# Optimization experiments

Measured on AMD Instinct MI355X. Metric: run time of the kernel, lower is better.

## Reference

```python
import jax, jax.numpy as jnp
import numpy as np

NEG_SLOPE = 0.2  # PyG GATConv default negative_slope


def gat_conv(x, edge_index, W, att_src, att_dst, bias):
    # PyG GATConv, heads=1, add_self_loops=True, lin bias=False, final bias added
    N = x.shape[0]
    h = x @ W                                     # [N, F]
    loops = jnp.arange(N, dtype=edge_index.dtype)
    src = jnp.concatenate([edge_index[0], loops])
    dst = jnp.concatenate([edge_index[1], loops])
    a_src = h @ att_src                           # [N]
    a_dst = h @ att_dst                           # [N]
    e = a_src[src] + a_dst[dst]
    e = jnp.where(e > 0, e, NEG_SLOPE * e)        # leaky_relu
    m = jax.ops.segment_max(e, dst, num_segments=N)
    w = jnp.exp(e - m[dst])
    denom = jax.ops.segment_sum(w, dst, num_segments=N)
    alpha = w / denom[dst]
    out = jax.ops.segment_sum(h[src] * alpha[:, None], dst, num_segments=N)
    return out + bias


def gcn_conv(x, edge_index, W, b):
    # PyG GCNConv: add self-loops + symmetric normalization
    N = x.shape[0]
    loops = jnp.arange(N, dtype=edge_index.dtype)
    src = jnp.concatenate([edge_index[0], loops])
    dst = jnp.concatenate([edge_index[1], loops])
    deg = jax.ops.segment_sum(jnp.ones(src.shape[0], dtype=x.dtype), dst, num_segments=N)
    dinv = jax.lax.rsqrt(jnp.maximum(deg, 1e-12))  # deg >= 1 thanks to self-loops
    norm = dinv[src] * dinv[dst]
    xw = x @ W
    return jax.ops.segment_sum(xw[src] * norm[:, None], dst, num_segments=N) + b


def get_final_node(x, batch, num_graphs):
    nn_ = jax.ops.segment_sum(jnp.ones(x.shape[0], dtype=jnp.int32), batch, num_segments=num_graphs)
    cum = jnp.concatenate([jnp.zeros(1, dtype=nn_.dtype), jnp.cumsum(nn_)[:-1]])
    return x[cum]


def ontology_emb(table, e1, e2, W, asrc, adst, b, idx_map):
    emb = gat_conv(table, e1, W, asrc, adst, b)
    emb = gat_conv(emb, e2, W, asrc, adst, b)
    return emb[idx_map]


def _forward(spec_emb, diag_table, proce_table, atc_table,
             diag_W, diag_asrc, diag_adst, diag_b,
             proce_W, proce_asrc, proce_adst, proce_b,
             atc_W, atc_asrc, atc_adst, atc_b,
             gcn_W1, gcn_b1, gcn_W2, gcn_b2, gcn_W3, gcn_b3,
             diag_e1, diag_e2, proce_e1, proce_e2, atc_e1, atc_e2,
             diag_map, proce_map, atc_map,
             left_x, left_graph_index, right_x, right_graph_index,
             left_x_batch, right_x_batch, num_graphs):
    diag_emb = ontology_emb(diag_table, diag_e1, diag_e2, diag_W, diag_asrc, diag_adst, diag_b, diag_map)
    proce_emb = ontology_emb(proce_table, proce_e1, proce_e2, proce_W, proce_asrc, proce_adst, proce_b, proce_map)
    atc_emb = ontology_emb(atc_table, atc_e1, atc_e2, atc_W, atc_asrc, atc_adst, atc_b, atc_map)
    all_emb = jnp.concatenate([spec_emb, diag_emb, proce_emb, atc_emb], axis=0)
    lh = all_emb[left_x[:, 0]]   # squeeze(dim=1)
    rh = all_emb[right_x[:, 0]]
    for W, b in ((gcn_W1, gcn_b1), (gcn_W2, gcn_b2), (gcn_W3, gcn_b3)):
        lh = gcn_conv(lh, left_graph_index, W, b)
        rh = gcn_conv(rh, right_graph_index, W, b)
    lf = get_final_node(lh, left_x_batch, num_graphs)
    rf = get_final_node(rh, right_x_batch, num_graphs)
    eps = 1e-6  # CosineSimilarity eps
    num = jnp.sum(lf * rf, axis=-1)
    den = jnp.maximum(jnp.linalg.norm(lf, axis=-1), eps) * jnp.maximum(jnp.linalg.norm(rf, axis=-1), eps)
    return num / den


def setup_inputs() -> dict:
    key = jax.random.key(0)
    ks = jax.random.split(key, 32)
    HID = 128
    B, NPG = 2048, 50
    N = B * NPG               # 102400 nodes per side
    E_PAT = 409600            # 4 edges per node
    DIAG_N, DIAG_L = 30000, 20000
    PROCE_N, PROCE_L = 12000, 8000
    ATC_N, ATC_L = 6000, 4000
    ALL = 1 + DIAG_L + PROCE_L + ATC_L
    f = lambda k, s: jax.random.normal(k, s, dtype=jnp.float32)
    scale = 0.1
    inp = {
        'spec_emb': f(ks[0], (1, HID)),
        'diag_table': f(ks[1], (DIAG_N, HID)),
        'proce_table': f(ks[2], (PROCE_N, HID)),
        'atc_table': f(ks[3], (ATC_N, HID)),
    }
    for i, nm in enumerate(['diag', 'proce', 'atc']):
        inp[nm + '_W'] = f(ks[4 + i], (HID, HID)) * scale
        inp[nm + '_asrc'] = f(ks[7 + i], (HID,)) * scale
        inp[nm + '_adst'] = f(ks[10 + i], (HID,)) * scale
        inp[nm + '_b'] = jnp.zeros((HID,), jnp.float32)
    for j in range(3):
        inp['gcn_W%d' % (j + 1)] = f(ks[13 + j], (HID, HID)) * scale
        inp['gcn_b%d' % (j + 1)] = jnp.zeros((HID,), jnp.float32)
    inp['diag_e1'] = jax.random.randint(ks[16], (2, DIAG_N), 0, DIAG_N, dtype=jnp.int32)
    inp['diag_e2'] = jax.random.randint(ks[17], (2, DIAG_N), 0, DIAG_N, dtype=jnp.int32)
    inp['proce_e1'] = jax.random.randint(ks[18], (2, PROCE_N), 0, PROCE_N, dtype=jnp.int32)
    inp['proce_e2'] = jax.random.randint(ks[19], (2, PROCE_N), 0, PROCE_N, dtype=jnp.int32)
    inp['atc_e1'] = jax.random.randint(ks[20], (2, ATC_N), 0, ATC_N, dtype=jnp.int32)
    inp['atc_e2'] = jax.random.randint(ks[21], (2, ATC_N), 0, ATC_N, dtype=jnp.int32)
    inp['diag_map'] = jnp.arange(DIAG_L, dtype=jnp.int32)
    inp['proce_map'] = jnp.arange(PROCE_L, dtype=jnp.int32)
    inp['atc_map'] = jnp.arange(ATC_L, dtype=jnp.int32)
    inp['left_x'] = jax.random.randint(ks[22], (N, 1), 0, ALL, dtype=jnp.int32)
    inp['right_x'] = jax.random.randint(ks[23], (N, 1), 0, ALL, dtype=jnp.int32)
    inp['left_graph_index'] = jax.random.randint(ks[24], (2, E_PAT), 0, N, dtype=jnp.int32)
    inp['right_graph_index'] = jax.random.randint(ks[25], (2, E_PAT), 0, N, dtype=jnp.int32)
    batch = jnp.repeat(jnp.arange(B, dtype=jnp.int32), NPG)
    inp['left_x_batch'] = batch
    inp['right_x_batch'] = batch
    inp['num_graphs'] = B
    return inp


def reference(spec_emb, diag_table, proce_table, atc_table,
              diag_W, diag_asrc, diag_adst, diag_b,
              proce_W, proce_asrc, proce_adst, proce_b,
              atc_W, atc_asrc, atc_adst, atc_b,
              gcn_W1, gcn_b1, gcn_W2, gcn_b2, gcn_W3, gcn_b3,
              diag_e1, diag_e2, proce_e1, proce_e2, atc_e1, atc_e2,
              diag_map, proce_map, atc_map,
              left_x, left_graph_index, right_x, right_graph_index,
              left_x_batch, right_x_batch, num_graphs):
    return _forward(spec_emb, diag_table, proce_table, atc_table,
                    diag_W, diag_asrc, diag_adst, diag_b,
                    proce_W, proce_asrc, proce_adst, proce_b,
                    atc_W, atc_asrc, atc_adst, atc_b,
                    gcn_W1, gcn_b1, gcn_W2, gcn_b2, gcn_W3, gcn_b3,
                    diag_e1, diag_e2, proce_e1, proce_e2, atc_e1, atc_e2,
                    diag_map, proce_map, atc_map,
                    left_x, left_graph_index, right_x, right_graph_index,
                    left_x_batch, right_x_batch, num_graphs)
```

## Files before the change

kernel.cpp:

```cpp
#include <hip/hip_runtime.h>
#include <hip/hip_bf16.h>

#define HID 128

typedef unsigned int uint;
typedef unsigned short ushort;
typedef short short8 __attribute__((ext_vector_type(8)));
typedef float f32x4 __attribute__((ext_vector_type(4)));

static inline int cdiv_i(long a, long b) { return (int)((a + b - 1) / b); }

__device__ __forceinline__ float bf2f(uint hi) {
    return __builtin_bit_cast(float, hi << 16);
}
__device__ __forceinline__ ushort f2bf(float f) {
    uint u = __builtin_bit_cast(uint, f);
    u = (u + 0x7fffu + ((u >> 16) & 1u)) >> 16;
    return (ushort)u;
}

__global__ void build_aug(const float* __restrict__ W1, const float* __restrict__ b1,
                          const float* __restrict__ b2,
                          float* __restrict__ aug1, float* __restrict__ aug2) {
    const int i = blockIdx.x * 256 + threadIdx.x;
    if (i < 128 * 128) aug1[i] = W1[i];
    else if (i < 129 * 128) aug1[i] = b1[i - 128 * 128];
    if (i < 128) aug2[129 * 128 + i] = b2[i];
}

__global__ void matmul128f(const float* __restrict__ A, const float* __restrict__ B,
                           float* __restrict__ C, int M) {
    const int idx = blockIdx.x * 256 + threadIdx.x;
    if (idx >= M * 128) return;
    const int i = idx >> 7, j = idx & 127;
    float s = 0.f;
#pragma unroll 8
    for (int k = 0; k < 128; ++k) s += A[i * 128 + k] * B[k * 128 + j];
    C[idx] = s;
}

struct W4 { const float* w[4]; };

__global__ void wtrans_k(W4 ws, ushort* __restrict__ out) {
    const int idx = blockIdx.x * 256 + threadIdx.x;
    if (idx >= 4 * 16384) return;
    const int m = idx >> 14;
    const int e = idx & 16383;
    const int n = e >> 7, k = e & 127;
    out[idx] = f2bf(ws.w[m][k * 128 + n]);
}

__device__ __forceinline__ void stage_wt(const ushort* __restrict__ Wt,
                                         ushort* __restrict__ wl) {
    const int t = threadIdx.x;
    const int row = t >> 1, half = (t & 1) * 64;
    const uint4* src = (const uint4*)(Wt + row * 128 + half);
    uint4* dst = (uint4*)(wl + row * 136 + half);
#pragma unroll
    for (int i = 0; i < 8; ++i) dst[i] = src[i];
}

template <typename AT>
__device__ __forceinline__ void load_afrag(const AT* __restrict__ A, long row,
                                           int koff, short8& af) {
    if constexpr (__is_same(AT, ushort)) {
        const uint4 raw = *(const uint4*)(A + row * 128 + koff);
        af = __builtin_bit_cast(short8, raw);
    } else {
        const float4* p = (const float4*)(A + row * 128 + koff);
        const float4 x0 = p[0], x1 = p[1];
        af[0] = (short)f2bf(x0.x); af[1] = (short)f2bf(x0.y);
        af[2] = (short)f2bf(x0.z); af[3] = (short)f2bf(x0.w);
        af[4] = (short)f2bf(x1.x); af[5] = (short)f2bf(x1.y);
        af[6] = (short)f2bf(x1.z); af[7] = (short)f2bf(x1.w);
    }
}

template <typename AT, typename OT>
__device__ __forceinline__ void mfma_tile(const AT* __restrict__ A,
                                          const ushort* __restrict__ wl,
                                          const float* __restrict__ bias,
                                          OT* __restrict__ C,
                                          long m0blk, long rowEnd) {
    const int tid = threadIdx.x;
    const int wave = tid >> 6, lane = tid & 63;
    const int r = lane & 15, q = lane >> 4;
    const long m0 = m0blk + wave * 32;

    f32x4 acc[2][8];
#pragma unroll
    for (int mi = 0; mi < 2; ++mi)
#pragma unroll
        for (int ni = 0; ni < 8; ++ni) acc[mi][ni] = (f32x4)0.f;

#pragma unroll
    for (int t = 0; t < 4; ++t) {
        const int koff = t * 32 + q * 8;
        short8 bfr[8];
#pragma unroll
        for (int ni = 0; ni < 8; ++ni) {
            const uint4 raw = *(const uint4*)(&wl[(ni * 16 + r) * 136 + koff]);
            bfr[ni] = __builtin_bit_cast(short8, raw);
        }
#pragma unroll
        for (int mi = 0; mi < 2; ++mi) {
            long row = m0 + mi * 16 + r;
            if (row >= rowEnd) row = rowEnd - 1;
            short8 af;
            load_afrag<AT>(A, row, koff, af);
#pragma unroll
            for (int ni = 0; ni < 8; ++ni)
                acc[mi][ni] = __builtin_amdgcn_mfma_f32_16x16x32_bf16(
                    af, bfr[ni], acc[mi][ni], 0, 0, 0);
        }
    }

#pragma unroll
    for (int mi = 0; mi < 2; ++mi) {
#pragma unroll
        for (int ni = 0; ni < 8; ++ni) {
            const int col = ni * 16 + r;
            const float bv = bias ? bias[col] : 0.f;
#pragma unroll
            for (int reg = 0; reg < 4; ++reg) {
                const long row = m0 + mi * 16 + q * 4 + reg;
                if (row < rowEnd) {
                    const float v = acc[mi][ni][reg] + bv;
                    if constexpr (__is_same(OT, ushort))
                        C[row * 128 + col] = f2bf(v);
                    else
                        C[row * 128 + col] = v;
                }
            }
        }
    }
}

template <typename OT>
__global__ __launch_bounds__(256) void gemm_gcn(const ushort* __restrict__ A,
                                                const ushort* __restrict__ Wt,
                                                const float* __restrict__ bias,
                                                OT* __restrict__ C, int M) {
    __shared__ ushort wl[128 * 136];
    stage_wt(Wt, wl);
    __syncthreads();
    const long m0 = (long)blockIdx.x * 256;
    mfma_tile<ushort, OT>(A, wl, bias, C, m0, M);
    if (m0 + 128 < M)
        mfma_tile<ushort, OT>(A, wl, bias, C, m0 + 128, M);
}

struct GOnto {
    const ushort* Wt0; const ushort* Wt1; const ushort* Wt2;
    const float* s0; const float* s1; const float* s2;
    const float* d0; const float* d1; const float* d2;
    int bs1, bs2;
    int r1, r2, r3;
};

template <typename AT>
__global__ __launch_bounds__(256) void gemm_onto(const AT* x0, const AT* x1,
                                                 const AT* x2, GOnto g,
                                                 ushort* __restrict__ H,
                                                 float* __restrict__ as_o,
                                                 float* __restrict__ ad_o) {
    __shared__ ushort wl[128 * 136];
    const int b = blockIdx.x;
    const int gid = (b >= g.bs1) + (b >= g.bs2);
    const ushort* Wt = (gid == 0) ? g.Wt0 : (gid == 1) ? g.Wt1 : g.Wt2;
    const float* avs = (gid == 0) ? g.s0 : (gid == 1) ? g.s1 : g.s2;
    const float* avd = (gid == 0) ? g.d0 : (gid == 1) ? g.d1 : g.d2;
    const AT* Ag = (gid == 0) ? x0 : (gid == 1) ? x1 : x2;
    const int bloc = b - ((gid == 0) ? 0 : (gid == 1) ? g.bs1 : g.bs2);
    const long rb = (gid == 0) ? 0 : (gid == 1) ? g.r1 : g.r2;
    const long Mg = ((gid == 0) ? g.r1 : (gid == 1) ? g.r2 : g.r3) - rb;
    stage_wt(Wt, wl);
    __syncthreads();

    const int tid = threadIdx.x;
    const int wave = tid >> 6, lane = tid & 63;
    const int r = lane & 15, q = lane >> 4;
    const long m0 = (long)bloc * 128 + wave * 32;

    f32x4 acc[2][8];
#pragma unroll
    for (int mi = 0; mi < 2; ++mi)
#pragma unroll
        for (int ni = 0; ni < 8; ++ni) acc[mi][ni] = (f32x4)0.f;

#pragma unroll
    for (int t = 0; t < 4; ++t) {
        const int koff = t * 32 + q * 8;
        short8 bfr[8];
#pragma unroll
        for (int ni = 0; ni < 8; ++ni) {
            const uint4 raw = *(const uint4*)(&wl[(ni * 16 + r) * 136 + koff]);
            bfr[ni] = __builtin_bit_cast(short8, raw);
        }
#pragma unroll
        for (int mi = 0; mi < 2; ++mi) {
            long row = m0 + mi * 16 + r;
            if (row >= Mg) row = Mg - 1;
            short8 af;
            load_afrag<AT>(Ag, row, koff, af);
#pragma unroll
            for (int ni = 0; ni < 8; ++ni)
                acc[mi][ni] = __builtin_amdgcn_mfma_f32_16x16x32_bf16(
                    af, bfr[ni], acc[mi][ni], 0, 0, 0);
        }
    }

    ushort* Hg = H + rb * 128;
#pragma unroll
    for (int mi = 0; mi < 2; ++mi) {
#pragma unroll
        for (int ni = 0; ni < 8; ++ni) {
            const int col = ni * 16 + r;
#pragma unroll
            for (int reg = 0; reg < 4; ++reg) {
                const long row = m0 + mi * 16 + q * 4 + reg;
                if (row < Mg) Hg[row * 128 + col] = f2bf(acc[mi][ni][reg]);
            }
        }
    }

    float asv[8], adv[8];
#pragma unroll
    for (int ni = 0; ni < 8; ++ni) {
        asv[ni] = avs[ni * 16 + r];
        adv[ni] = avd[ni * 16 + r];
    }
#pragma unroll
    for (int mi = 0; mi < 2; ++mi) {
#pragma unroll
        for (int reg = 0; reg < 4; ++reg) {
            float ps = 0.f, pd = 0.f;
#pragma unroll
            for (int ni = 0; ni < 8; ++ni) {
                ps += acc[mi][ni][reg] * asv[ni];
                pd += acc[mi][ni][reg] * adv[ni];
            }
#pragma unroll
            for (int o = 1; o < 16; o <<= 1) {
                ps += __shfl_xor(ps, o);
                pd += __shfl_xor(pd, o);
            }
            const long row = m0 + mi * 16 + q * 4 + reg;
            if (r == 0 && row < Mg) {
                as_o[rb + row] = ps;
                ad_o[rb + row] = pd;
            }
        }
    }
}

struct GatP {
    int r1, r2;
    int ob0, ob1, ob2;
    const float* b0; const float* b1; const float* b2;
};

__device__ __forceinline__ void acc8(float* acc, float w, const uint4 v) {
    acc[0] += w * bf2f(v.x & 0xffff);
    acc[1] += w * bf2f(v.x >> 16);
    acc[2] += w * bf2f(v.y & 0xffff);
    acc[3] += w * bf2f(v.y >> 16);
    acc[4] += w * bf2f(v.z & 0xffff);
    acc[5] += w * bf2f(v.z >> 16);
    acc[6] += w * bf2f(v.w & 0xffff);
    acc[7] += w * bf2f(v.w >> 16);
}

__global__ __launch_bounds__(256) void gat_all(const ushort* __restrict__ h,
                                               const float* __restrict__ as,
                                               const float* __restrict__ ad,
                                               const int* __restrict__ offs,
                                               const int* __restrict__ srcl,
                                               GatP p, ushort* __restrict__ out,
                                               int Mtot) {
    const int node = blockIdx.x * 16 + (threadIdx.x >> 4);
    const int ql = threadIdx.x & 15;
    if (node >= Mtot) return;
    const int gid = (node >= p.r1) + (node >= p.r2);
    const int rb = (gid == 0) ? 0 : (gid == 1) ? p.r1 : p.r2;
    const int ob = (gid == 0) ? p.ob0 : (gid == 1) ? p.ob1 : p.ob2;
    const float* bias = (gid == 0) ? p.b0 : (gid == 1) ? p.b1 : p.b2;
    const int local = node - rb;
    const int beg = offs[ob + local], end = offs[ob + local + 1];
    const float adv = ad[node];
    float m = -1e30f;
    for (int j = beg; j < end; ++j) {
        float e = as[rb + srcl[j]] + adv;
        e = (e > 0.f) ? e : 0.2f * e;
        m = fmaxf(m, e);
    }
    float denom = 0.f;
    float acc[8] = {0.f, 0.f, 0.f, 0.f, 0.f, 0.f, 0.f, 0.f};
    int j = beg;
    for (; j + 2 <= end; j += 2) {
        const int s0 = srcl[j], s1 = srcl[j + 1];
        float e0 = as[rb + s0] + adv; e0 = (e0 > 0.f) ? e0 : 0.2f * e0;
        float e1 = as[rb + s1] + adv; e1 = (e1 > 0.f) ? e1 : 0.2f * e1;
        const float w0 = __expf(e0 - m), w1 = __expf(e1 - m);
        const uint4 v0 = *(const uint4*)(h + (size_t)(rb + s0) * 128 + ql * 8);
        const uint4 v1 = *(const uint4*)(h + (size_t)(rb + s1) * 128 + ql * 8);
        denom += w0 + w1;
        acc8(acc, w0, v0);
        acc8(acc, w1, v1);
    }
    if (j < end) {
        const int s0 = srcl[j];
        float e0 = as[rb + s0] + adv; e0 = (e0 > 0.f) ? e0 : 0.2f * e0;
        const float w0 = __expf(e0 - m);
        const uint4 v0 = *(const uint4*)(h + (size_t)(rb + s0) * 128 + ql * 8);
        denom += w0;
        acc8(acc, w0, v0);
    }
    const float inv = 1.f / denom;
    const float4 bv0 = *(const float4*)(bias + ql * 8);
    const float4 bv1 = *(const float4*)(bias + ql * 8 + 4);
    uint4 o;
    o.x = (uint)f2bf(acc[0] * inv + bv0.x) | ((uint)f2bf(acc[1] * inv + bv0.y) << 16);
    o.y = (uint)f2bf(acc[2] * inv + bv0.z) | ((uint)f2bf(acc[3] * inv + bv0.w) << 16);
    o.z = (uint)f2bf(acc[4] * inv + bv1.x) | ((uint)f2bf(acc[5] * inv + bv1.y) << 16);
    o.w = (uint)f2bf(acc[6] * inv + bv1.z) | ((uint)f2bf(acc[7] * inv + bv1.w) << 16);
    *(uint4*)(out + (size_t)node * 128 + ql * 8) = o;
}

struct CsrDesc {
    const int* esrc[8];
    const int* edst[8];
    int ebase[9];
    int nbase[9];
    int totE;
};

__global__ void csr_count_b(CsrDesc d, int* __restrict__ cnt, int* __restrict__ pos) {
    const int i = blockIdx.x * 256 + threadIdx.x;
    if (i >= d.totE) return;
    int li = 0;
#pragma unroll
    for (int k = 1; k < 8; ++k) li += (i >= d.ebase[k]);
    const int v = d.nbase[li] + d.edst[li][i - d.ebase[li]];
    pos[i] = atomicAdd(&cnt[v], 1);
}

__global__ void csr_fill_b(CsrDesc d, const int* __restrict__ offs,
                           const int* __restrict__ pos, const int* __restrict__ cnt,
                           int* __restrict__ srcl, int4* __restrict__ pedge,
                           const float* __restrict__ dinv,
                           const int* __restrict__ lx, const int* __restrict__ rx,
                           int NP, int NV, int pB) {
    const int i = blockIdx.x * 256 + threadIdx.x;
    int v, s, li, idx;
    if (i < d.totE) {
        li = 0;
#pragma unroll
        for (int k = 1; k < 8; ++k) li += (i >= d.ebase[k]);
        const int j = i - d.ebase[li];
        v = d.nbase[li] + d.edst[li][j];
        s = d.esrc[li][j];
        idx = offs[v] + pos[i];
    } else if (i < d.totE + NV) {
        v = i - d.totE;
        li = 0;
#pragma unroll
        for (int k = 1; k < 8; ++k) li += (v >= d.nbase[k]);
        s = v - d.nbase[li];
        idx = offs[v] + cnt[v];
    } else return;
    if (li >= 6) {
        const int sg = (li - 6) * NP + s;
        int4 rec;
        rec.x = sg;
        rec.y = (li == 7 ? rx : lx)[s];
        rec.z = __float_as_int(dinv[v - d.nbase[6]] * dinv[sg]);
        rec.w = 0;
        pedge[idx - pB] = rec;
    } else {
        srcl[idx] = s;
    }
}

__global__ void first_node(const int* __restrict__ bL, const int* __restrict__ bR,
                           int NP, int* __restrict__ gfL, int* __restrict__ gfR) {
    const int i = blockIdx.x * 256 + threadIdx.x;
    if (i >= 2 * NP) return;
    const int side = i >= NP;
    const int ii = i - (side ? NP : 0);
    const int* b = side ? bR : bL;
    int* gf = side ? gfR : gfL;
    const int cur = b[ii];
    const int prev = (ii == 0) ? -1 : b[ii - 1];
    for (int g = prev + 1; g <= cur; ++g) gf[g] = ii;
}

__global__ __launch_bounds__(1024) void scan_tile(const int* __restrict__ in,
                                                  int* __restrict__ out,
                                                  int* __restrict__ bsum, int n,
                                                  int pn0, int pcnt,
                                                  float* __restrict__ dinv) {
    __shared__ int buf[1024];
    const int tid = threadIdx.x;
    const int i = blockIdx.x * 1024 + tid;
    const int v = (i < n) ? (in[i] + 1) : 0;
    if (i >= pn0 && i < pn0 + pcnt)
        dinv[i - pn0] = rsqrtf(fmaxf((float)v, 1e-12f));
    buf[tid] = v;
    __syncthreads();
    int x = v;
    for (int o = 1; o < 1024; o <<= 1) {
        const int t = (tid >= o) ? buf[tid - o] : 0;
        __syncthreads();
        x += t;
        buf[tid] = x;
        __syncthreads();
    }
    if (i < n) out[i] = x - v;
    if (tid == 1023) bsum[blockIdx.x] = x;
}

__global__ __launch_bounds__(1024) void scan_single(int* __restrict__ bsum, int nb) {
    __shared__ int buf[1024];
    const int tid = threadIdx.x;
    const int v = (tid < nb) ? bsum[tid] : 0;
    buf[tid] = v;
    __syncthreads();
    int x = v;
    for (int o = 1; o < 1024; o <<= 1) {
        const int t = (tid >= o) ? buf[tid - o] : 0;
        __syncthreads();
        x += t;
        buf[tid] = x;
        __syncthreads();
    }
    if (tid < nb) bsum[tid] = x - v;
    if (tid == 1023) bsum[nb] = x;
}

__global__ void scan_add(int* __restrict__ out, const int* __restrict__ bsum,
                         int n, int nb) {
    const int i = blockIdx.x * 256 + threadIdx.x;
    if (i < n) out[i] += bsum[i >> 10];
    else if (i == n) out[i] = bsum[nb];
}

struct EmbD {
    const float* spec; const ushort* oE;
    const int* m0; const int* m1; const int* m2;
    int lb2, lb3;
    int r1, r2;
    long ALLr;
};

__global__ void build_emb(EmbD d, ushort* __restrict__ out) {
    const long t = (long)blockIdx.x * 256 + threadIdx.x;
    if (t >= d.ALLr * 16) return;
    const int row = (int)(t >> 4), c = (int)(t & 15);
    uint4 o;
    if (row == 0) {
        const float4 f0 = ((const float4*)d.spec)[c * 2];
        const float4 f1 = ((const float4*)d.spec)[c * 2 + 1];
        o.x = (uint)f2bf(f0.x) | ((uint)f2bf(f0.y) << 16);
        o.y = (uint)f2bf(f0.z) | ((uint)f2bf(f0.w) << 16);
        o.z = (uint)f2bf(f1.x) | ((uint)f2bf(f1.y) << 16);
        o.w = (uint)f2bf(f1.z) | ((uint)f2bf(f1.w) << 16);
    } else {
        const int seg = (row >= d.lb2) + (row >= d.lb3);
        const int local = row - ((seg == 0) ? 1 : (seg == 1) ? d.lb2 : d.lb3);
        const int* mp = (seg == 0) ? d.m0 : (seg == 1) ? d.m1 : d.m2;
        const int rb = (seg == 0) ? 0 : (seg == 1) ? d.r1 : d.r2;
        o = ((const uint4*)(d.oE + (size_t)(rb + mp[local]) * 128))[c];
    }
    ((uint4*)out)[(size_t)row * 16 + c] = o;
}

__global__ __launch_bounds__(256) void gcn_agg1(const ushort* __restrict__ A3,
                                                const int4* __restrict__ pedge,
                                                const int* __restrict__ offs6,
                                                const float* __restrict__ c1,
                                                ushort* __restrict__ t1,
                                                int NP2, int pB) {
    const int n2 = blockIdx.x * 16 + (threadIdx.x >> 4);
    const int ql = threadIdx.x & 15;
    if (n2 >= NP2) return;
    const int beg = offs6[n2] - pB, end = offs6[n2 + 1] - pB;
    float acc[8] = {0.f, 0.f, 0.f, 0.f, 0.f, 0.f, 0.f, 0.f};
    int j = beg;
    for (; j + 2 <= end; j += 2) {
        const int4 r0 = pedge[j], r1 = pedge[j + 1];
        const float w0 = __int_as_float(r0.z), w1 = __int_as_float(r1.z);
        const uint4 v0 = *(const uint4*)(A3 + (size_t)r0.y * 128 + ql * 8);
        const uint4 v1 = *(const uint4*)(A3 + (size_t)r1.y * 128 + ql * 8);
        acc8(acc, w0, v0);
        acc8(acc, w1, v1);
    }
    if (j < end) {
        const int4 r0 = pedge[j];
        const uint4 v0 = *(const uint4*)(A3 + (size_t)r0.y * 128 + ql * 8);
        acc8(acc, __int_as_float(r0.z), v0);
    }
    const float4 bv0 = *(const float4*)(c1 + ql * 8);
    const float4 bv1 = *(const float4*)(c1 + ql * 8 + 4);
    uint4 o;
    o.x = (uint)f2bf(acc[0] + bv0.x) | ((uint)f2bf(acc[1] + bv0.y) << 16);
    o.y = (uint)f2bf(acc[2] + bv0.z) | ((uint)f2bf(acc[3] + bv0.w) << 16);
    o.z = (uint)f2bf(acc[4] + bv1.x) | ((uint)f2bf(acc[5] + bv1.y) << 16);
    o.w = (uint)f2bf(acc[6] + bv1.z) | ((uint)f2bf(acc[7] + bv1.w) << 16);
    *(uint4*)(t1 + (size_t)n2 * 128 + ql * 8) = o;
}

__device__ __forceinline__ void gcn_q_acc(const ushort* __restrict__ x,
                                          const int4* __restrict__ pedge,
                                          int beg, int end, int ql, float* acc) {
    int j = beg;
    for (; j + 2 <= end; j += 2) {
        const int4 r0 = pedge[j], r1 = pedge[j + 1];
        const float w0 = __int_as_float(r0.z), w1 = __int_as_float(r1.z);
        const uint4 v0 = *(const uint4*)(x + (size_t)r0.x * 128 + ql * 8);
        const uint4 v1 = *(const uint4*)(x + (size_t)r1.x * 128 + ql * 8);
        acc8(acc, w0, v0);
        acc8(acc, w1, v1);
    }
    if (j < end) {
        const int4 r0 = pedge[j];
        const uint4 v0 = *(const uint4*)(x + (size_t)r0.x * 128 + ql * 8);
        acc8(acc, __int_as_float(r0.z), v0);
    }
}

__global__ __launch_bounds__(256) void gcn_agg2(const ushort* __restrict__ t1,
                                                const int4* __restrict__ pedge,
                                                const int* __restrict__ offs6,
                                                const float* __restrict__ c2,
                                                ushort* __restrict__ t2,
                                                int NP2, int pB) {
    const int n2 = blockIdx.x * 16 + (threadIdx.x >> 4);
    const int ql = threadIdx.x & 15;
    if (n2 >= NP2) return;
    const int beg = offs6[n2] - pB, end = offs6[n2 + 1] - pB;
    float acc[8] = {0.f, 0.f, 0.f, 0.f, 0.f, 0.f, 0.f, 0.f};
    gcn_q_acc(t1, pedge, beg, end, ql, acc);
    const float4 bv0 = *(const float4*)(c2 + ql * 8);
    const float4 bv1 = *(const float4*)(c2 + ql * 8 + 4);
    uint4 o;
    o.x = (uint)f2bf(acc[0] + bv0.x) | ((uint)f2bf(acc[1] + bv0.y) << 16);
    o.y = (uint)f2bf(acc[2] + bv0.z) | ((uint)f2bf(acc[3] + bv0.w) << 16);
    o.z = (uint)f2bf(acc[4] + bv1.x) | ((uint)f2bf(acc[5] + bv1.y) << 16);
    o.w = (uint)f2bf(acc[6] + bv1.z) | ((uint)f2bf(acc[7] + bv1.w) << 16);
    *(uint4*)(t2 + (size_t)n2 * 128 + ql * 8) = o;
}

__global__ __launch_bounds__(256) void gcn_final(const ushort* __restrict__ t2,
                                                 const int4* __restrict__ pedge,
                                                 const int* __restrict__ offs6,
                                                 const int* __restrict__ gfL,
                                                 const int* __restrict__ gfR,
                                                 const float* __restrict__ b3,
                                                 float* __restrict__ lfrf,
                                                 int B, int NP, int pB) {
    const int g2 = blockIdx.x * 16 + (threadIdx.x >> 4);
    const int ql = threadIdx.x & 15;
    if (g2 >= 2 * B) return;
    const int side = g2 >= B;
    const int gl = g2 - (side ? B : 0);
    const int n2 = (side ? NP : 0) + (side ? gfR : gfL)[gl];
    const int beg = offs6[n2] - pB, end = offs6[n2 + 1] - pB;
    float acc[8] = {0.f, 0.f, 0.f, 0.f, 0.f, 0.f, 0.f, 0.f};
    gcn_q_acc(t2, pedge, beg, end, ql, acc);
    const float4 bv0 = *(const float4*)(b3 + ql * 8);
    const float4 bv1 = *(const float4*)(b3 + ql * 8 + 4);
    float* op = lfrf + (size_t)g2 * 128 + ql * 8;
    op[0] = acc[0] + bv0.x; op[1] = acc[1] + bv0.y;
    op[2] = acc[2] + bv0.z; op[3] = acc[3] + bv0.w;
    op[4] = acc[4] + bv1.x; op[5] = acc[5] + bv1.y;
    op[6] = acc[6] + bv1.z; op[7] = acc[7] + bv1.w;
}

__global__ __launch_bounds__(256) void cosine_k(const float* __restrict__ lfrf,
                                                float* __restrict__ out, int B) {
    const int g = blockIdx.x * 4 + (threadIdx.x >> 6);
    const int lane = threadIdx.x & 63;
    if (g >= B) return;
    const float2 a = *(const float2*)(lfrf + (size_t)g * 128 + lane * 2);
    const float2 b = *(const float2*)(lfrf + (size_t)(B + g) * 128 + lane * 2);
    float num = a.x * b.x + a.y * b.y;
    float na = a.x * a.x + a.y * a.y;
    float nb = b.x * b.x + b.y * b.y;
#pragma unroll
    for (int o = 32; o > 0; o >>= 1) {
        num += __shfl_down(num, o);
        na += __shfl_down(na, o);
        nb += __shfl_down(nb, o);
    }
    if (lane == 0)
        out[g] = num / (fmaxf(sqrtf(na), 1e-6f) * fmaxf(sqrtf(nb), 1e-6f));
}

extern "C" void kernel_launch(void* const* d_in, const int* in_sizes, int n_in,
                              void* d_out, int out_size, void* d_ws, size_t ws_size,
                              hipStream_t stream) {
    (void)n_in; (void)ws_size;
    const float* spec = (const float*)d_in[0];
    const float* tabs[3] = {(const float*)d_in[1], (const float*)d_in[2], (const float*)d_in[3]};
    const float* ontW[3] = {(const float*)d_in[4], (const float*)d_in[8], (const float*)d_in[12]};
    const float* ontAs[3] = {(const float*)d_in[5], (const float*)d_in[9], (const float*)d_in[13]};
    const float* ontAd[3] = {(const float*)d_in[6], (const float*)d_in[10], (const float*)d_in[14]};
    const float* ontB[3] = {(const float*)d_in[7], (const float*)d_in[11], (const float*)d_in[15]};
    const float* gcnW[3] = {(const float*)d_in[16], (const float*)d_in[18], (const float*)d_in[20]};
    const float* gcnB[3] = {(const float*)d_in[17], (const float*)d_in[19], (const float*)d_in[21]};
    const int* e1s[3] = {(const int*)d_in[22], (const int*)d_in[24], (const int*)d_in[26]};
    const int* e2s[3] = {(const int*)d_in[23], (const int*)d_in[25], (const int*)d_in[27]};
    const int* maps[3] = {(const int*)d_in[28], (const int*)d_in[29], (const int*)d_in[30]};
    const int* left_x = (const int*)d_in[31];
    const int* right_x = (const int*)d_in[32];
    const int* left_eg = (const int*)d_in[33];
    const int* right_eg = (const int*)d_in[34];
    const int* left_batch = (const int*)d_in[35];
    const int* right_batch = (const int*)d_in[36];

    int Ms[3] = {in_sizes[1] / HID, in_sizes[2] / HID, in_sizes[3] / HID};
    int E1s[3] = {in_sizes[22] / 2, in_sizes[24] / 2, in_sizes[26] / 2};
    int E2s[3] = {in_sizes[23] / 2, in_sizes[25] / 2, in_sizes[27] / 2};
    int Ls[3] = {in_sizes[28], in_sizes[29], in_sizes[30]};
    const int NP = in_sizes[31];
    const int EP = in_sizes[33] / 2;
    const int B = out_size;
    const long ALL = 1 + (long)Ls[0] + Ls[1] + Ls[2];
    const int Mtot = Ms[0] + Ms[1] + Ms[2];
    const int r1 = Ms[0], r2 = Ms[0] + Ms[1];

    CsrDesc dsc;
    int eCnt[8], nCnt[8];
    for (int i = 0; i < 3; ++i) {
        dsc.esrc[2 * i] = e1s[i];     dsc.edst[2 * i] = e1s[i] + E1s[i];
        dsc.esrc[2 * i + 1] = e2s[i]; dsc.edst[2 * i + 1] = e2s[i] + E2s[i];
        eCnt[2 * i] = E1s[i]; eCnt[2 * i + 1] = E2s[i];
        nCnt[2 * i] = Ms[i];  nCnt[2 * i + 1] = Ms[i];
    }
    dsc.esrc[6] = left_eg;  dsc.edst[6] = left_eg + EP;  eCnt[6] = EP; nCnt[6] = NP;
    dsc.esrc[7] = right_eg; dsc.edst[7] = right_eg + EP; eCnt[7] = EP; nCnt[7] = NP;
    dsc.ebase[0] = 0;
    int nb_acc = 0;
    for (int i = 0; i < 8; ++i) {
        dsc.ebase[i + 1] = dsc.ebase[i] + eCnt[i];
        dsc.nbase[i] = nb_acc;
        nb_acc += nCnt[i];
    }
    const int NV = nb_acc;
    dsc.nbase[8] = NV;
    dsc.totE = dsc.ebase[8];
    const int totEntries = dsc.totE + NV;
    const int pB = dsc.ebase[6] + dsc.nbase[6];
    const int pEntries = totEntries - pB;

    char* ws = (char*)d_ws;
    size_t off = 0;
    auto alloc = [&](size_t bytes) -> void* {
        off = (off + 255) & ~(size_t)255;
        void* p = ws + off;
        off += bytes;
        return p;
    };
    ushort* wt4 = (ushort*)alloc((size_t)4 * 16384 * 2);
    float* aug1 = (float*)alloc((size_t)130 * 128 * 4);
    float* aug2 = (float*)alloc((size_t)130 * 128 * 4);
    float* Pout = (float*)alloc((size_t)130 * 128 * 4);
    ushort* allemb = (ushort*)alloc((size_t)ALL * HID * 2);
    ushort* A3 = (ushort*)alloc((size_t)ALL * HID * 2);
    float* lfrf = (float*)alloc((size_t)2 * B * HID * 4);
    int* cnt = (int*)alloc((size_t)NV * 4);
    int* offs = (int*)alloc((size_t)(NV + 1) * 4);
    int* pos = (int*)alloc((size_t)dsc.totE * 4);
    int* srcl = (int*)alloc((size_t)pB * 4);
    int4* pedge = (int4*)alloc((size_t)pEntries * 16);
    int* bsum = (int*)alloc(1025 * 4);
    float* dinv = (float*)alloc((size_t)2 * NP * 4);
    float* as = (float*)alloc((size_t)Mtot * 4);
    float* ad = (float*)alloc((size_t)Mtot * 4);
    int* gfL = (int*)alloc((size_t)(B + 1) * 4);
    int* gfR = (int*)alloc((size_t)(B + 1) * 4);
    ushort* t1 = (ushort*)alloc((size_t)2 * NP * HID * 2);
    ushort* big = (ushort*)alloc((size_t)2 * NP * HID * 2);
    ushort* hbuf = big;
    ushort* obuf = big + (size_t)Mtot * HID;
    ushort* t2 = big;

    build_aug<<<cdiv_i(129 * 128, 256), 256, 0, stream>>>(gcnW[0], gcnB[0], gcnB[1],
                                                          aug1, aug2);
    matmul128f<<<cdiv_i(129 * 128, 256), 256, 0, stream>>>(aug1, gcnW[1], aug2, 129);
    matmul128f<<<cdiv_i(130 * 128, 256), 256, 0, stream>>>(aug2, gcnW[2], Pout, 130);
    const float* c1 = Pout + 128 * 128;
    const float* c2 = Pout + 129 * 128;

    W4 w4;
    w4.w[0] = ontW[0]; w4.w[1] = ontW[1]; w4.w[2] = ontW[2]; w4.w[3] = Pout;
    wtrans_k<<<cdiv_i(4 * 16384, 256), 256, 0, stream>>>(w4, wt4);
    const ushort* wtOnt[3] = {wt4, wt4 + 16384, wt4 + 2 * 16384};
    const ushort* WpT = wt4 + 3 * 16384;

    hipMemsetAsync(cnt, 0, (size_t)NV * 4, stream);
    csr_count_b<<<cdiv_i(dsc.totE, 256), 256, 0, stream>>>(dsc, cnt, pos);
    {
        const int nb = cdiv_i(NV, 1024);
        scan_tile<<<nb, 1024, 0, stream>>>(cnt, offs, bsum, NV, dsc.nbase[6],
                                           2 * NP, dinv);
        scan_single<<<1, 1024, 0, stream>>>(bsum, nb);
        scan_add<<<cdiv_i(NV + 1, 256), 256, 0, stream>>>(offs, bsum, NV, nb);
    }
    csr_fill_b<<<cdiv_i(totEntries, 256), 256, 0, stream>>>(dsc, offs, pos, cnt,
                                                            srcl, pedge, dinv,
                                                            left_x, right_x,
                                                            NP, NV, pB);
    first_node<<<cdiv_i(2 * NP, 256), 256, 0, stream>>>(left_batch, right_batch,
                                                        NP, gfL, gfR);

    GOnto go;
    go.Wt0 = wtOnt[0]; go.Wt1 = wtOnt[1]; go.Wt2 = wtOnt[2];
    go.s0 = ontAs[0]; go.s1 = ontAs[1]; go.s2 = ontAs[2];
    go.d0 = ontAd[0]; go.d1 = ontAd[1]; go.d2 = ontAd[2];
    go.bs1 = cdiv_i(Ms[0], 128);
    go.bs2 = go.bs1 + cdiv_i(Ms[1], 128);
    const int totBlk = go.bs2 + cdiv_i(Ms[2], 128);
    go.r1 = r1; go.r2 = r2; go.r3 = Mtot;

    for (int layer = 0; layer < 2; ++layer) {
        const GatP gp{r1, r2,
                      dsc.nbase[0 + layer], dsc.nbase[2 + layer], dsc.nbase[4 + layer],
                      ontB[0], ontB[1], ontB[2]};
        if (layer == 0)
            gemm_onto<float><<<totBlk, 256, 0, stream>>>(tabs[0], tabs[1], tabs[2],
                                                         go, hbuf, as, ad);
        else
            gemm_onto<ushort><<<totBlk, 256, 0, stream>>>(
                obuf, obuf + (size_t)r1 * HID, obuf + (size_t)r2 * HID,
                go, hbuf, as, ad);
        gat_all<<<cdiv_i(Mtot, 16), 256, 0, stream>>>(hbuf, as, ad, offs, srcl, gp,
                                                      obuf, Mtot);
    }

    EmbD ed;
    ed.spec = spec; ed.oE = obuf;
    ed.m0 = maps[0]; ed.m1 = maps[1]; ed.m2 = maps[2];
    ed.lb2 = 1 + Ls[0]; ed.lb3 = 1 + Ls[0] + Ls[1];
    ed.r1 = r1; ed.r2 = r2; ed.ALLr = ALL;
    build_emb<<<cdiv_i(ALL * 16, 256), 256, 0, stream>>>(ed, allemb);

    const int* offs6 = offs + dsc.nbase[6];
    gemm_gcn<ushort><<<cdiv_i(ALL, 256), 256, 0, stream>>>(
        allemb, WpT, nullptr, A3, (int)ALL);
    gcn_agg1<<<cdiv_i(2 * NP, 16), 256, 0, stream>>>(A3, pedge, offs6,
                                                     c1, t1, 2 * NP, pB);
    gcn_agg2<<<cdiv_i(2 * NP, 16), 256, 0, stream>>>(t1, pedge, offs6,
                                                     c2, t2, 2 * NP, pB);
    gcn_final<<<cdiv_i(2 * B, 16), 256, 0, stream>>>(t2, pedge, offs6, gfL, gfR,
                                                     gcnB[2], lfrf, B, NP, pB);

    cosine_k<<<cdiv_i(B, 4), 256, 0, stream>>>(lfrf, (float*)d_out, B);
}
```

Baseline: 409.7 us.

## Restrict GCN aggregation to nodes reachable from graph first nodes

Only the first node of each graph is read at the output, so the change marks the nodes that feed it. It marks 1-hop and 2-hop in-neighbours of those first nodes with atomic bitmask passes over the edges and builds compacted node lists. The first two GCN aggregation layers then process only listed nodes, and csr_fill skips writing edge records for unmarked destinations. This cuts gather work in gcn_agg1/agg2 at the cost of two extra edge-scan kernels, atomics, and memsets; the reduction depends on how many nodes are within two hops of a first node.

```diff
diff --git a/kernel.cpp b/kernel.cpp
--- a/kernel.cpp
+++ b/kernel.cpp
@@ -350,6 +350,7 @@
                            int* __restrict__ srcl, int4* __restrict__ pedge,
                            const float* __restrict__ dinv,
                            const int* __restrict__ lx, const int* __restrict__ rx,
+                           const int* __restrict__ mk,
                            int NP, int NV, int pB) {
     const int i = blockIdx.x * 256 + threadIdx.x;
     int v, s, li, idx;
@@ -370,11 +371,13 @@
         idx = offs[v] + cnt[v];
     } else return;
     if (li >= 6) {
+        const int n2l = v - d.nbase[6];
+        if (mk[n2l] == 0) return;
         const int sg = (li - 6) * NP + s;
         int4 rec;
         rec.x = sg;
         rec.y = (li == 7 ? rx : lx)[s];
-        rec.z = __float_as_int(dinv[v - d.nbase[6]] * dinv[sg]);
+        rec.z = __float_as_int(dinv[n2l] * dinv[sg]);
         rec.w = 0;
         pedge[idx - pB] = rec;
     } else {
@@ -383,7 +386,8 @@
 }
 
 __global__ void first_node(const int* __restrict__ bL, const int* __restrict__ bR,
-                           int NP, int* __restrict__ gfL, int* __restrict__ gfR) {
+                           int NP, int* __restrict__ gfL, int* __restrict__ gfR,
+                           int* __restrict__ mk) {
     const int i = blockIdx.x * 256 + threadIdx.x;
     if (i >= 2 * NP) return;
     const int side = i >= NP;
@@ -392,7 +396,33 @@
     int* gf = side ? gfR : gfL;
     const int cur = b[ii];
     const int prev = (ii == 0) ? -1 : b[ii - 1];
-    for (int g = prev + 1; g <= cur; ++g) gf[g] = ii;
+    if (cur > prev) {
+        for (int g = prev + 1; g <= cur; ++g) gf[g] = ii;
+        mk[i] = 1;
+    }
+}
+
+__device__ __forceinline__ void try_append(int* __restrict__ mk, int bit, int n,
+                                           int* __restrict__ list, int* __restrict__ cnt) {
+    if ((atomicOr(&mk[n], bit) & bit) == 0)
+        list[atomicAdd(cnt, 1)] = n;
+}
+
+__global__ void mark_k(const int* __restrict__ lEg, const int* __restrict__ rEg,
+                       int EP, int NP, int* __restrict__ mk, int testBit, int setBit,
+                       int* __restrict__ list, int* __restrict__ cnt) {
+    const int i = blockIdx.x * 256 + threadIdx.x;
+    int src, dst;
+    if (i < 2 * EP) {
+        const int side = i >= EP;
+        const int e = i - side * EP;
+        const int* eg = side ? rEg : lEg;
+        src = side * NP + eg[e];
+        dst = side * NP + eg[EP + e];
+    } else if (i < 2 * EP + 2 * NP) {
+        src = dst = i - 2 * EP;
+    } else return;
+    if (mk[dst] & testBit) try_append(mk, setBit, src, list, cnt);
 }
 
 __global__ __launch_bounds__(1024) void scan_tile(const int* __restrict__ in,
@@ -480,10 +510,12 @@
                                                 const int* __restrict__ offs6,
                                                 const float* __restrict__ c1,
                                                 ushort* __restrict__ t1,
-                                                int NP2, int pB) {
-    const int n2 = blockIdx.x * 16 + (threadIdx.x >> 4);
+                                                const int* __restrict__ list1,
+                                                const int* __restrict__ cnt1, int pB) {
+    const int id = blockIdx.x * 16 + (threadIdx.x >> 4);
     const int ql = threadIdx.x & 15;
-    if (n2 >= NP2) return;
+    if (id >= *cnt1) return;
+    const int n2 = list1[id];
     const int beg = offs6[n2] - pB, end = offs6[n2 + 1] - pB;
     float acc[8] = {0.f, 0.f, 0.f, 0.f, 0.f, 0.f, 0.f, 0.f};
     int j = beg;
@@ -534,10 +566,12 @@
                                                 const int* __restrict__ offs6,
                                                 const float* __restrict__ c2,
                                                 ushort* __restrict__ t2,
-                                                int NP2, int pB) {
-    const int n2 = blockIdx.x * 16 + (threadIdx.x >> 4);
+                                                const int* __restrict__ list2,
+                                                const int* __restrict__ cnt2, int pB) {
+    const int id = blockIdx.x * 16 + (threadIdx.x >> 4);
     const int ql = threadIdx.x & 15;
-    if (n2 >= NP2) return;
+    if (id >= *cnt2) return;
+    const int n2 = list2[id];
     const int beg = offs6[n2] - pB, end = offs6[n2 + 1] - pB;
     float acc[8] = {0.f, 0.f, 0.f, 0.f, 0.f, 0.f, 0.f, 0.f};
     gcn_q_acc(t1, pedge, beg, end, ql, acc);
@@ -680,6 +714,10 @@
     float* ad = (float*)alloc((size_t)Mtot * 4);
     int* gfL = (int*)alloc((size_t)(B + 1) * 4);
     int* gfR = (int*)alloc((size_t)(B + 1) * 4);
+    int* mk = (int*)alloc((size_t)2 * NP * 4);
+    int* list1 = (int*)alloc((size_t)2 * NP * 4);
+    int* list2 = (int*)alloc((size_t)2 * NP * 4);
+    int* cnt12 = (int*)alloc(2 * 4);
     ushort* t1 = (ushort*)alloc((size_t)2 * NP * HID * 2);
     ushort* big = (ushort*)alloc((size_t)2 * NP * HID * 2);
     ushort* hbuf = big;
@@ -698,6 +736,15 @@
     wtrans_k<<<cdiv_i(4 * 16384, 256), 256, 0, stream>>>(w4, wt4);
     const ushort* wtOnt[3] = {wt4, wt4 + 16384, wt4 + 2 * 16384};
     const ushort* WpT = wt4 + 3 * 16384;
+
+    hipMemsetAsync(mk, 0, (size_t)2 * NP * 4, stream);
+    hipMemsetAsync(cnt12, 0, 2 * 4, stream);
+    first_node<<<cdiv_i(2 * NP, 256), 256, 0, stream>>>(left_batch, right_batch,
+                                                        NP, gfL, gfR, mk);
+    mark_k<<<cdiv_i(2 * EP + 2 * NP, 256), 256, 0, stream>>>(
+        left_eg, right_eg, EP, NP, mk, 1, 2, list2, cnt12 + 1);
+    mark_k<<<cdiv_i(2 * EP + 2 * NP, 256), 256, 0, stream>>>(
+        left_eg, right_eg, EP, NP, mk, 2, 4, list1, cnt12 + 0);
 
     hipMemsetAsync(cnt, 0, (size_t)NV * 4, stream);
     csr_count_b<<<cdiv_i(dsc.totE, 256), 256, 0, stream>>>(dsc, cnt, pos);
@@ -710,10 +757,8 @@
     }
     csr_fill_b<<<cdiv_i(totEntries, 256), 256, 0, stream>>>(dsc, offs, pos, cnt,
                                                             srcl, pedge, dinv,
-                                                            left_x, right_x,
+                                                            left_x, right_x, mk,
                                                             NP, NV, pB);
-    first_node<<<cdiv_i(2 * NP, 256), 256, 0, stream>>>(left_batch, right_batch,
-                                                        NP, gfL, gfR);
 
     GOnto go;
     go.Wt0 = wtOnt[0]; go.Wt1 = wtOnt[1]; go.Wt2 = wtOnt[2];
@@ -749,10 +794,10 @@
     const int* offs6 = offs + dsc.nbase[6];
     gemm_gcn<ushort><<<cdiv_i(ALL, 256), 256, 0, stream>>>(
         allemb, WpT, nullptr, A3, (int)ALL);
-    gcn_agg1<<<cdiv_i(2 * NP, 16), 256, 0, stream>>>(A3, pedge, offs6,
-                                                     c1, t1, 2 * NP, pB);
-    gcn_agg2<<<cdiv_i(2 * NP, 16), 256, 0, stream>>>(t1, pedge, offs6,
-                                                     c2, t2, 2 * NP, pB);
+    gcn_agg1<<<cdiv_i(2 * NP, 16), 256, 0, stream>>>(A3, pedge, offs6, c1, t1,
+                                                     list1, cnt12 + 0, pB);
+    gcn_agg2<<<cdiv_i(2 * NP, 16), 256, 0, stream>>>(t1, pedge, offs6, c2, t2,
+                                                     list2, cnt12 + 1, pB);
     gcn_final<<<cdiv_i(2 * B, 16), 256, 0, stream>>>(t2, pedge, offs6, gfL, gfR,
                                                      gcnB[2], lfrf, B, NP, pB);
 
```

After: 678.4 us. 1.66x slower.
